# Kernel optimization log

Hardware: AMD Instinct MI355X
Metric: run time of the kernel (lower is better)

## Reference

```python
import jax, jax.numpy as jnp
import numpy as np

N = 10000       # nodes (cells)
NFEAT = 2000    # gene-expression features
NFE = 256       # embed features
NH = 128        # nhid
NHE = 64        # nhid_embed
L = 2           # gcn_hid_layers_num
NOUT = 20       # output classes
BN_EPS = 1e-5


def bn_eval(x, g, b, rm, rv):
    # BatchNorm1d in eval mode: affine with running stats
    return g * (x - rm) / jnp.sqrt(rv + BN_EPS) + b


def lstm_layer(seq, Wih, Whh, bih, bhh):
    # seq: [T, N, H_in]; PyTorch gate order i, f, g, o
    Hd = Whh.shape[1]
    def step(carry, xt):
        h, c = carry
        z = xt @ Wih.T + h @ Whh.T + bih + bhh  # [N, 4H]
        i, f, g, o = jnp.split(z, 4, axis=1)
        c = jax.nn.sigmoid(f) * c + jax.nn.sigmoid(i) * jnp.tanh(g)
        h = jax.nn.sigmoid(o) * jnp.tanh(c)
        return (h, c), h
    h0 = jnp.zeros((seq.shape[1], Hd), seq.dtype)
    _, hs = jax.lax.scan(step, (h0, h0), seq)
    return hs  # [T, N, H]


def setup_inputs() -> dict:
    key = jax.random.key(0)
    ks = iter(jax.random.split(key, 48))
    def rn(shape, scale=1.0):
        return jax.random.normal(next(ks), shape, dtype=jnp.float32) * scale
    inp = {}
    inp["x"] = rn((N, NFEAT))
    inp["embed"] = rn((N, NFE))
    inp["adj"] = jax.random.uniform(next(ks), (N, N), dtype=jnp.float32)
    inp["W_in"] = rn((NH, NFEAT), NFEAT ** -0.5); inp["b_in"] = jnp.zeros((NH,), jnp.float32)
    inp["bn_in_g"] = jnp.ones((NH,), jnp.float32); inp["bn_in_b"] = jnp.zeros((NH,), jnp.float32)
    inp["bn_in_rm"] = rn((NH,), 0.1); inp["bn_in_rv"] = jnp.ones((NH,), jnp.float32)
    # gs_block: Linear(2*nhid -> nhid) per layer (concat self + mean-aggregated neighbors)
    inp["W_gs"] = rn((L, NH, 2 * NH), (2 * NH) ** -0.5); inp["b_gs"] = jnp.zeros((L, NH), jnp.float32)
    for l in range(2):  # 2-layer LSTM jumping-knowledge
        inp[f"Wih{l}"] = rn((4 * NH, NH), NH ** -0.5)
        inp[f"Whh{l}"] = rn((4 * NH, NH), NH ** -0.5)
        inp[f"bih{l}"] = jnp.zeros((4 * NH,), jnp.float32)
        inp[f"bhh{l}"] = jnp.zeros((4 * NH,), jnp.float32)
    inp["W_emb"] = rn((NHE, NFE), NFE ** -0.5); inp["b_emb"] = jnp.zeros((NHE,), jnp.float32)
    inp["bn_emb_g"] = jnp.ones((NHE,), jnp.float32); inp["bn_emb_b"] = jnp.zeros((NHE,), jnp.float32)
    inp["bn_emb_rm"] = rn((NHE,), 0.1); inp["bn_emb_rv"] = jnp.ones((NHE,), jnp.float32)
    D = NH + NHE
    inp["W_fc"] = rn((D, D), D ** -0.5); inp["b_fc"] = jnp.zeros((D,), jnp.float32)
    inp["bn_fc_g"] = jnp.ones((D,), jnp.float32); inp["bn_fc_b"] = jnp.zeros((D,), jnp.float32)
    inp["bn_fc_rm"] = rn((D,), 0.1); inp["bn_fc_rv"] = jnp.ones((D,), jnp.float32)
    inp["W_out"] = rn((NOUT, D), D ** -0.5); inp["b_out"] = jnp.zeros((NOUT,), jnp.float32)
    return inp


def _forward(x, embed, adj, W_in, b_in, bn_in_g, bn_in_b, bn_in_rm, bn_in_rv,
             W_gs, b_gs, Wih0, Whh0, bih0, bhh0, Wih1, Whh1, bih1, bhh1,
             W_emb, b_emb, bn_emb_g, bn_emb_b, bn_emb_rm, bn_emb_rv,
             W_fc, b_fc, bn_fc_g, bn_fc_b, bn_fc_rm, bn_fc_rv, W_out, b_out):
    # input projection + BN + ELU (dropout: eval mode -> no-op)
    h = jax.nn.elu(bn_eval(x @ W_in.T + b_in, bn_in_g, bn_in_b, bn_in_rm, bn_in_rv))
    # GraphSAGE mean aggregator: row-normalized dense adjacency
    adj_norm = adj / adj.sum(1, keepdims=True)
    jk = []
    for l in range(L):
        neigh = adj_norm @ h                              # [N, NH] neighbor mean
        comb = jnp.concatenate([h, neigh], axis=1)        # [N, 2NH] (gcn=False)
        h = jax.nn.relu(comb @ W_gs[l].T + b_gs[l])
        h = h / jnp.maximum(jnp.linalg.norm(h, axis=1, keepdims=True), 1e-12)  # F.normalize
        jk.append(h)
    seq = jnp.stack(jk, 0)                                # [L, N, NH]
    hs = lstm_layer(seq, Wih0, Whh0, bih0, bhh0)
    hs = lstm_layer(hs, Wih1, Whh1, bih1, bhh1)
    h = hs.mean(0)                                        # JK: mean of LSTM outputs
    h = jax.nn.elu(bn_eval(h, bn_in_g, bn_in_b, bn_in_rm, bn_in_rv))  # bn_node_in_exp reused
    e = jax.nn.elu(bn_eval(embed @ W_emb.T + b_emb, bn_emb_g, bn_emb_b, bn_emb_rm, bn_emb_rv))
    h = jnp.concatenate([h, e], axis=1)                   # [N, NH+NHE]
    h = jax.nn.elu(bn_eval(h @ W_fc.T + b_fc, bn_fc_g, bn_fc_b, bn_fc_rm, bn_fc_rv))
    logits = h @ W_out.T + b_out
    return jax.nn.log_softmax(logits, axis=1)


def reference(x, embed, adj, W_in, b_in, bn_in_g, bn_in_b, bn_in_rm, bn_in_rv,
              W_gs, b_gs, Wih0, Whh0, bih0, bhh0, Wih1, Whh1, bih1, bhh1,
              W_emb, b_emb, bn_emb_g, bn_emb_b, bn_emb_rm, bn_emb_rv,
              W_fc, b_fc, bn_fc_g, bn_fc_b, bn_fc_rm, bn_fc_rv, W_out, b_out):
    return _forward(x, embed, adj, W_in, b_in, bn_in_g, bn_in_b, bn_in_rm, bn_in_rv,
                    W_gs, b_gs, Wih0, Whh0, bih0, bhh0, Wih1, Whh1, bih1, bhh1,
                    W_emb, b_emb, bn_emb_g, bn_emb_b, bn_emb_rm, bn_emb_rv,
                    W_fc, b_fc, bn_fc_g, bn_fc_b, bn_fc_rm, bn_fc_rv, W_out, b_out)
```

## Files before the change

### kernel.cpp

```cpp
#include <hip/hip_runtime.h>
#include <hip/hip_bf16.h>
#include <math.h>

#define N_NODES 10000
#define NFEAT   2000
#define NFE     256
#define NH      128
#define NHE     64
#define NOUT    20
#define DCAT    192
#define BN_EPS  1e-5f

#define KP      10016
#define KSTEPS  313
#define MT      157
#define NSPLIT  8
#define KC      40
#define MPAD    10048

typedef __attribute__((ext_vector_type(8))) short  bf16x8;
typedef __attribute__((ext_vector_type(4))) float  f32x4;

__device__ __forceinline__ float sigm(float x) { return 1.0f / (1.0f + expf(-x)); }

__device__ __forceinline__ unsigned short f2bf(float x) {
    union { __hip_bfloat16 h; unsigned short u; } c;
    c.h = __float2bfloat16(x);
    return c.u;
}

__device__ __forceinline__ bf16x8 cvt8(const float* v) {
    bf16x8 r;
    #pragma unroll
    for (int i = 0; i < 8; ++i) r[i] = (short)f2bf(v[i]);
    return r;
}

__global__ __launch_bounds__(256) void htrans_kernel(const float* __restrict__ h,
                                                     unsigned short* __restrict__ hT)
{
    __shared__ float t[32][36];
    const int k0 = blockIdx.x * 32, c0 = blockIdx.y * 32;
    {
        int r = threadIdx.x >> 3, ci = threadIdx.x & 7;
        int kg = k0 + r;
        float4 v = {0.f, 0.f, 0.f, 0.f};
        if (kg < N_NODES) v = *(const float4*)(h + (size_t)kg * NH + c0 + ci * 4);
        t[r][ci * 4 + 0] = v.x; t[r][ci * 4 + 1] = v.y;
        t[r][ci * 4 + 2] = v.z; t[r][ci * 4 + 3] = v.w;
    }
    __syncthreads();
    {
        int c = threadIdx.x >> 3, ki = threadIdx.x & 7;
        ushort4 o;
        o.x = f2bf(t[ki * 4 + 0][c]); o.y = f2bf(t[ki * 4 + 1][c]);
        o.z = f2bf(t[ki * 4 + 2][c]); o.w = f2bf(t[ki * 4 + 3][c]);
        *(ushort4*)(hT + (size_t)(c0 + c) * KP + k0 + ki * 4) = o;
    }
}

__global__ __launch_bounds__(256) void adjmm_kernel(const float* __restrict__ adj,
                                                    const unsigned short* __restrict__ hT,
                                                    float* __restrict__ part,
                                                    float* __restrict__ part_s)
{
    __shared__ unsigned short sa[64 * 32];
    __shared__ unsigned short sb[128 * 32];
    const int tid  = threadIdx.x;
    const int lane = tid & 63, w = tid >> 6;
    const int m0   = blockIdx.x * 64;
    const int ks0  = blockIdx.y * KC;
    const int ks1  = min(ks0 + KC, KSTEPS);
    const int r0   = (w & 1) * 32;
    const int c0   = (w >> 1) * 64;

    const int arow = tid >> 2, agrp = tid & 3;
    const size_t abase = (size_t)min(m0 + arow, N_NODES - 1) * N_NODES;
    const int bcol = tid >> 1, bg0 = (tid & 1) * 2;

    float rs = 0.f;
// ... 32 lines not shown
            int g   = lane >> 4;
            av[rb] = *(const bf16x8*)(sa + row * 32 + ((g ^ (row & 3)) << 3));
        }
        #pragma unroll
        for (int cb = 0; cb < 4; ++cb) {
            int col = c0 + cb * 16 + (lane & 15);
            int g   = lane >> 4;
            bv[cb] = *(const bf16x8*)(sb + col * 32 + ((g ^ (col & 3)) << 3));
        }
        #pragma unroll
        for (int rb = 0; rb < 2; ++rb)
            #pragma unroll
            for (int cb = 0; cb < 4; ++cb)
                acc[rb][cb] = __builtin_amdgcn_mfma_f32_16x16x32_bf16(av[rb], bv[cb],
                                                                      acc[rb][cb], 0, 0, 0);
    }

    rs += __shfl_xor(rs, 1);
    rs += __shfl_xor(rs, 2);
    if ((tid & 3) == 0) part_s[(size_t)blockIdx.y * MPAD + m0 + arow] = rs;

    float* pout = part + (size_t)blockIdx.y * MPAD * NH;
    #pragma unroll
    for (int rb = 0; rb < 2; ++rb) {
        #pragma unroll
        for (int cb = 0; cb < 4; ++cb) {
            int rowb = m0 + r0 + rb * 16 + (lane >> 4) * 4;
            int col  = c0 + cb * 16 + (lane & 15);
            #pragma unroll
            for (int reg = 0; reg < 4; ++reg)
                pout[(size_t)(rowb + reg) * NH + col] = acc[rb][cb][reg];
        }
    }
}

__global__ __launch_bounds__(256) void sinv_kernel(const float* __restrict__ part_s,
                                                   float* __restrict__ sinv)
{
    int m = blockIdx.x * 256 + threadIdx.x;
    if (m >= N_NODES) return;
    float a = 0.f;
    #pragma unroll
    for (int c = 0; c < NSPLIT; ++c) a += part_s[(size_t)c * MPAD + m];
    sinv[m] = 1.0f / a;
}

__global__ __launch_bounds__(256) void nreduce_kernel(const float* __restrict__ part,
                                                      const float* __restrict__ sinv,
                                                      float* __restrict__ neigh)
{
    int idx = blockIdx.x * 256 + threadIdx.x;
    if (idx >= N_NODES * NH / 4) return;
    const int m = idx >> 5;
    const size_t ch = (size_t)MPAD * NH / 4;
    const float4* p = (const float4*)part;
    float a0 = 0.f, a1 = 0.f, a2 = 0.f, a3 = 0.f;
    #pragma unroll
    for (int c = 0; c < NSPLIT; ++c) {
        float4 v = p[c * ch + idx];
        a0 += v.x; a1 += v.y; a2 += v.z; a3 += v.w;
    }
    const float inv = sinv[m];
    float4 o; o.x = a0 * inv; o.y = a1 * inv; o.z = a2 * inv; o.w = a3 * inv;
    *(float4*)(neigh + (size_t)idx * 4) = o;
}

__global__ __launch_bounds__(256) void xw_mfma_kernel(const float* __restrict__ x,
                                                      const float* __restrict__ Wn,
                                                      float* __restrict__ part)
{
    __shared__ unsigned short sa[64 * 32];
    __shared__ unsigned short sb[128 * 32];
    const int tid  = threadIdx.x;
    const int lane = tid & 63, w = tid >> 6;
    const int m0   = blockIdx.x * 64;
    const int TOT  = (NFEAT + 31) / 32;
    const int s0   = blockIdx.y * 8;
    const int s1   = min(s0 + 8, TOT);
    const int r0   = (w & 1) * 32;
    const int c0   = (w >> 1) * 64;

    const int arow = tid >> 2, agrp = tid & 3;
    const size_t abase = (size_t)min(m0 + arow, N_NODES - 1) * NFEAT;

    f32x4 acc[2][4];
    #pragma unroll
    for (int i = 0; i < 2; ++i)
        #pragma unroll
        for (int j = 0; j < 4; ++j) acc[i][j] = (f32x4){0.f, 0.f, 0.f, 0.f};

    for (int ks = s0; ks < s1; ++ks) {
        const int k0 = ks * 32;
        float av8[8], bv8[2][8];
        {
            const int kg = k0 + agrp * 8;
            if (kg + 8 <= NFEAT) {
                float4 u0 = *(const float4*)(x + abase + kg);
                float4 u1 = *(const float4*)(x + abase + kg + 4);
                av8[0]=u0.x; av8[1]=u0.y; av8[2]=u0.z; av8[3]=u0.w;
                av8[4]=u1.x; av8[5]=u1.y; av8[6]=u1.z; av8[7]=u1.w;
            } else {
// ... 44 lines not shown
            for (int cb = 0; cb < 4; ++cb)
                acc[rb][cb] = __builtin_amdgcn_mfma_f32_16x16x32_bf16(av[rb], bv[cb],
                                                                      acc[rb][cb], 0, 0, 0);
    }
    float* pout = part + (size_t)blockIdx.y * MPAD * NH;
    #pragma unroll
    for (int rb = 0; rb < 2; ++rb)
        #pragma unroll
        for (int cb = 0; cb < 4; ++cb) {
            int rowb = m0 + r0 + rb * 16 + (lane >> 4) * 4;
            int col  = c0 + cb * 16 + (lane & 15);
            #pragma unroll
            for (int reg = 0; reg < 4; ++reg)
                pout[(size_t)(rowb + reg) * NH + col] = acc[rb][cb][reg];
        }
}

__global__ __launch_bounds__(256) void xw_reduce_kernel(const float* __restrict__ part,
                                                        const float* __restrict__ bias,
                                                        const float* __restrict__ g,
                                                        const float* __restrict__ bb,
                                                        const float* __restrict__ rm,
                                                        const float* __restrict__ rv,
                                                        float* __restrict__ h)
{
    int idx = blockIdx.x * 256 + threadIdx.x;
    if (idx >= N_NODES * NH / 4) return;
    const int c4 = (idx & 31) * 4;
    const size_t ch = (size_t)MPAD * NH / 4;
    const float4* p = (const float4*)part;
    float a[4] = {0.f, 0.f, 0.f, 0.f};
    #pragma unroll
    for (int c = 0; c < NSPLIT; ++c) {
        float4 v = p[c * ch + idx];
        a[0] += v.x; a[1] += v.y; a[2] += v.z; a[3] += v.w;
    }
    float o[4];
    #pragma unroll
    for (int j = 0; j < 4; ++j) {
        int c = c4 + j;
        float sc = g[c] / sqrtf(rv[c] + BN_EPS);
        float t = (a[j] + bias[c] - rm[c]) * sc + bb[c];
        o[j] = t > 0.f ? t : expm1f(t);
    }
    float4 ov; ov.x = o[0]; ov.y = o[1]; ov.z = o[2]; ov.w = o[3];
    *(float4*)(h + (size_t)idx * 4) = ov;
}

template<int BM, int BN, int EPI>
__global__ __launch_bounds__(256) void wgemm_mfma_kernel(
    int M, int K, int kSplitA,
    const float* __restrict__ a1, int lda1,
    const float* __restrict__ a2, int lda2,
    int kSplitB,
    const float* __restrict__ b1, int ldb1,
    const float* __restrict__ b2, int ldb2,
    float* __restrict__ out, int ldo,
    const float* __restrict__ bias1, const float* __restrict__ bias2,
    const float* __restrict__ bng, const float* __restrict__ bnb,
    const float* __restrict__ bnrm, const float* __restrict__ bnrv)
{
    constexpr int WC = BN / 64;
    constexpr int WR = 4 / WC;
    static_assert(WR * WC == 4 && BM == WR * 32, "geometry");
    constexpr int NGA = BM * 4 / 256;
    constexpr int NGB = BN * 4 / 256;
    __shared__ unsigned short sa[BM * 32];
    __shared__ unsigned short sb[BN * 32];
    const int tid  = threadIdx.x;
    const int lane = tid & 63, w = tid >> 6;
    const int m0   = blockIdx.x * BM, n0 = blockIdx.y * BN;
    const int r0   = (w % WR) * 32, c0 = (w / WR) * 64;

    f32x4 acc[2][4];
    #pragma unroll
    for (int i = 0; i < 2; ++i)
        #pragma unroll
        for (int j = 0; j < 4; ++j) acc[i][j] = (f32x4){0.f, 0.f, 0.f, 0.f};

    for (int k0 = 0; k0 < K; k0 += 32) {
        float ar[NGA][8], br[NGB][8];
        #pragma unroll
        for (int t = 0; t < NGA; ++t) {
            int gidx = tid + t * 256;
            int row = gidx >> 2, grp = gidx & 3;
            int mg = min(m0 + row, M - 1);
            int kg = k0 + grp * 8;
            const float* src = (kg < kSplitA) ? (a1 + (size_t)mg * lda1 + kg)
                                              : (a2 + (size_t)mg * lda2 + (kg - kSplitA));
            float4 u0 = *(const float4*)src;
            float4 u1 = *(const float4*)(src + 4);
            ar[t][0]=u0.x; ar[t][1]=u0.y; ar[t][2]=u0.z; ar[t][3]=u0.w;
            ar[t][4]=u1.x; ar[t][5]=u1.y; ar[t][6]=u1.z; ar[t][7]=u1.w;
        }
        #pragma unroll
        for (int t = 0; t < NGB; ++t) {
            int gidx = tid + t * 256;
            int n = gidx >> 2, grp = gidx & 3;
            int ng = n0 + n;
            int kg = k0 + grp * 8;
            const float* src = (kg < kSplitB) ? (b1 + (size_t)ng * ldb1 + kg)
                                              : (b2 + (size_t)ng * ldb2 + (kg - kSplitB));
            float4 u0 = *(const float4*)src;
            float4 u1 = *(const float4*)(src + 4);
            br[t][0]=u0.x; br[t][1]=u0.y; br[t][2]=u0.z; br[t][3]=u0.w;
            br[t][4]=u1.x; br[t][5]=u1.y; br[t][6]=u1.z; br[t][7]=u1.w;
        }
        __syncthreads();
        #pragma unroll
        for (int t = 0; t < NGA; ++t) {
            int gidx = tid + t * 256;
            int row = gidx >> 2, grp = gidx & 3;
            *(bf16x8*)(sa + row * 32 + ((grp ^ (row & 3)) << 3)) = cvt8(ar[t]);
        }
        #pragma unroll
        for (int t = 0; t < NGB; ++t) {
            int gidx = tid + t * 256;
            int n = gidx >> 2, grp = gidx & 3;
            *(bf16x8*)(sb + n * 32 + ((grp ^ (n & 3)) << 3)) = cvt8(br[t]);
        }
        __syncthreads();
        bf16x8 av[2], bv[4];
        #pragma unroll
        for (int rb = 0; rb < 2; ++rb) {
            int row = r0 + rb * 16 + (lane & 15);
            int g   = lane >> 4;
            av[rb] = *(const bf16x8*)(sa + row * 32 + ((g ^ (row & 3)) << 3));
        }
        #pragma unroll
        for (int cb = 0; cb < 4; ++cb) {
            int col = c0 + cb * 16 + (lane & 15);
            int g   = lane >> 4;
            bv[cb] = *(const bf16x8*)(sb + col * 32 + ((g ^ (col & 3)) << 3));
        }
        #pragma unroll
        for (int rb = 0; rb < 2; ++rb)
            #pragma unroll
            for (int cb = 0; cb < 4; ++cb)
                acc[rb][cb] = __builtin_amdgcn_mfma_f32_16x16x32_bf16(av[rb], bv[cb],
                                                                      acc[rb][cb], 0, 0, 0);
    }

    #pragma unroll
    for (int cb = 0; cb < 4; ++cb) {
        const int colg = n0 + c0 + cb * 16 + (lane & 15);
        float badd = bias1[colg];
        if constexpr (EPI == 0) badd += bias2[colg];
        float sc = 0.f, sh = 0.f;
        if constexpr (EPI == 1) {
            sc = bng[colg] / sqrtf(bnrv[colg] + BN_EPS);
            sh = bnb[colg] - bnrm[colg] * sc;
        }
        #pragma unroll
        for (int rb = 0; rb < 2; ++rb) {
            int rowb = m0 + r0 + rb * 16 + (lane >> 4) * 4;
            #pragma unroll
            for (int reg = 0; reg < 4; ++reg) {
                int m = rowb + reg;
                if (m < M) {
                    float t = acc[rb][cb][reg] + badd;
                    if constexpr (EPI == 1) {
                        t = t * sc + sh;
                        t = t > 0.f ? t : expm1f(t);
                    }
                    if constexpr (EPI == 2) t = fmaxf(t, 0.f);
                    out[(size_t)m * ldo + colg] = t;
                }
            }
        }
    }
}

__global__ __launch_bounds__(256) void rownorm_kernel(const float* __restrict__ in,
                                                      float* __restrict__ out)
{
    const int w = threadIdx.x >> 6, lane = threadIdx.x & 63;
    const int r = blockIdx.x * 4 + w;
    float2 v = ((const float2*)(in + (size_t)r * NH))[lane];
    float ss = v.x * v.x + v.y * v.y;
    #pragma unroll
    for (int msk = 32; msk >= 1; msk >>= 1) ss += __shfl_xor(ss, msk);
    float sc = 1.0f / fmaxf(sqrtf(ss), 1e-12f);
    float2 o; o.x = v.x * sc; o.y = v.y * sc;
    ((float2*)(out + (size_t)r * NH))[lane] = o;
}

template<bool HASC>
__global__ __launch_bounds__(256) void lstm_gate_kernel(const float* __restrict__ z,
                                                        const float* __restrict__ cprev,
                                                        float* __restrict__ hout,
                                                        float* __restrict__ cout)
{
    int idx = blockIdx.x * 256 + threadIdx.x;
    if (idx >= N_NODES * NH / 4) return;
    int m = idx >> 5, c4 = (idx & 31) * 4;
    const float* zr = z + (size_t)m * 512 + c4;
    float4 zi = *(const float4*)(zr);
    float4 zf = *(const float4*)(zr + 128);
    float4 zg = *(const float4*)(zr + 256);
    float4 zo = *(const float4*)(zr + 384);
    float4 cp = {0.f, 0.f, 0.f, 0.f};
    if (HASC) cp = *(const float4*)(cprev + (size_t)m * NH + c4);
    float zia[4] = {zi.x, zi.y, zi.z, zi.w};
    float zfa[4] = {zf.x, zf.y, zf.z, zf.w};
    float zga[4] = {zg.x, zg.y, zg.z, zg.w};
    float zoa[4] = {zo.x, zo.y, zo.z, zo.w};
    float cpa[4] = {cp.x, cp.y, cp.z, cp.w};
    float ho[4], co[4];
    #pragma unroll
    for (int j = 0; j < 4; ++j) {
        float ig = sigm(zia[j]);
        float gg = tanhf(zga[j]);
        float cn = ig * gg;
        if (HASC) cn += sigm(zfa[j]) * cpa[j];
        co[j] = cn;
        ho[j] = sigm(zoa[j]) * tanhf(cn);
    }
    float4 hv; hv.x = ho[0]; hv.y = ho[1]; hv.z = ho[2]; hv.w = ho[3];
    float4 cv; cv.x = co[0]; cv.y = co[1]; cv.z = co[2]; cv.w = co[3];
    *(float4*)(hout + (size_t)m * NH + c4) = hv;
    *(float4*)(cout + (size_t)m * NH + c4) = cv;
}

__global__ __launch_bounds__(256) void jkmean_bnelu_kernel(const float* __restrict__ a,
                                                           const float* __restrict__ b,
                                                           const float* __restrict__ g,
                                                           const float* __restrict__ bb,
                                                           const float* __restrict__ rm,
                                                           const float* __restrict__ rv,
                                                           float* __restrict__ out)
{
    int idx = blockIdx.x * 256 + threadIdx.x;
    if (idx >= N_NODES * NH / 4) return;
    int c4 = (idx & 31) * 4;
    float4 va = *(const float4*)(a + (size_t)idx * 4);
    float4 vb = *(const float4*)(b + (size_t)idx * 4);
    float av[4] = {va.x, va.y, va.z, va.w};
    float bv[4] = {vb.x, vb.y, vb.z, vb.w};
    float o[4];
    #pragma unroll
    for (int j = 0; j < 4; ++j) {
        int c = c4 + j;
        float t = 0.5f * (av[j] + bv[j]);
        float sc = g[c] / sqrtf(rv[c] + BN_EPS);
        t = (t - rm[c]) * sc + bb[c];
        o[j] = t > 0.f ? t : expm1f(t);
    }
    float4 ov; ov.x = o[0]; ov.y = o[1]; ov.z = o[2]; ov.w = o[3];
    *(float4*)(out + (size_t)idx * 4) = ov;
}

__global__ __launch_bounds__(256) void out_kernel(const float* __restrict__ hfc,
                                                  const float* __restrict__ W_out,
                                                  const float* __restrict__ b_out,
                                                  float* __restrict__ out)
{
    __shared__ float wl[NOUT * 193];
    __shared__ float rl[4][DCAT];
    const int tid = threadIdx.x;
    for (int i = tid; i < NOUT * DCAT; i += 256)
        wl[(i / DCAT) * 193 + (i % DCAT)] = W_out[i];
    const int w = tid >> 6, lane = tid & 63;
    const int r = blockIdx.x * 4 + w;
    for (int k = lane; k < DCAT; k += 64) rl[w][k] = hfc[(size_t)r * DCAT + k];
    __syncthreads();
    const int c = lane;
    float acc = -INFINITY;
    if (c < NOUT) {
        acc = b_out[c];
        #pragma unroll 4
        for (int k = 0; k < DCAT; ++k) acc += rl[w][k] * wl[c * 193 + k];
    }
// ... 35 lines not shown
    const float* bn_e_g  = (const float*)d_in[21];
    const float* bn_e_b  = (const float*)d_in[22];
    const float* bn_e_rm = (const float*)d_in[23];
    const float* bn_e_rv = (const float*)d_in[24];
    const float* W_fc    = (const float*)d_in[25];
    const float* b_fc    = (const float*)d_in[26];
    const float* bn_f_g  = (const float*)d_in[27];
    const float* bn_f_b  = (const float*)d_in[28];
    const float* bn_f_rm = (const float*)d_in[29];
    const float* bn_f_rv = (const float*)d_in[30];
    const float* W_out   = (const float*)d_in[31];
    const float* b_out   = (const float*)d_in[32];
    float* outp = (float*)d_out;

    const size_t HB = (size_t)N_NODES * NH * sizeof(float);
    char* wp = (char*)d_ws;
    auto carve = [&](size_t bytes) {
        void* p = (void*)wp;
        wp += (bytes + 1023) & ~(size_t)1023;
        return p;
    };
    float* part  = (float*)carve((size_t)NSPLIT * MPAD * NH * sizeof(float));
    float* part_s= (float*)carve((size_t)NSPLIT * MPAD * sizeof(float));
    float* sinv  = (float*)carve(N_NODES * sizeof(float));
    float* h_in  = (float*)carve(HB);
    float* neigh = (float*)carve(HB);
    float* jkraw = (float*)carve(HB);
    float* jk0   = (float*)carve(HB);
    float* jk1   = (float*)carve(HB);
    float* h1_0  = (float*)carve(HB);
    float* h1_1  = (float*)carve(HB);
    float* c1    = (float*)carve(HB);
    float* h2_0  = (float*)carve(HB);
    float* h2_1  = (float*)carve(HB);
    float* c2    = (float*)carve(HB);
    float* hpost = (float*)carve(HB);
    float* z     = (float*)carve((size_t)N_NODES * 512 * sizeof(float));
    float* e     = (float*)carve((size_t)N_NODES * NHE * sizeof(float));
    float* hfc   = (float*)carve((size_t)N_NODES * DCAT * sizeof(float));
    unsigned short* hT = (unsigned short*)carve((size_t)NH * KP * 2);
    if ((size_t)(wp - (char*)d_ws) > ws_size) return;

    const dim3 blk(256);

    xw_mfma_kernel<<<dim3(MT, 8), blk, 0, stream>>>(x, W_in, part);
    xw_reduce_kernel<<<1250, blk, 0, stream>>>(part, b_in, bn_in_g, bn_in_b,
                                               bn_in_rm, bn_in_rv, h_in);

    htrans_kernel<<<dim3(KSTEPS, 4), blk, 0, stream>>>(h_in, hT);
    adjmm_kernel<<<dim3(MT, NSPLIT), blk, 0, stream>>>(adj, hT, part, part_s);
    sinv_kernel<<<40, blk, 0, stream>>>(part_s, sinv);
    nreduce_kernel<<<1250, blk, 0, stream>>>(part, sinv, neigh);
    wgemm_mfma_kernel<64, 128, 2><<<dim3(MT, 1), blk, 0, stream>>>(
        N_NODES, 2 * NH, NH, h_in, NH, neigh, NH,
        2 * NH, W_gs, 2 * NH, nullptr, 0,
        jkraw, NH, b_gs, nullptr, nullptr, nullptr, nullptr, nullptr);
    rownorm_kernel<<<2500, blk, 0, stream>>>(jkraw, jk0);

    htrans_kernel<<<dim3(KSTEPS, 4), blk, 0, stream>>>(jk0, hT);
    adjmm_kernel<<<dim3(MT, NSPLIT), blk, 0, stream>>>(adj, hT, part, part_s);
    sinv_kernel<<<40, blk, 0, stream>>>(part_s, sinv);
    nreduce_kernel<<<1250, blk, 0, stream>>>(part, sinv, neigh);
    wgemm_mfma_kernel<64, 128, 2><<<dim3(MT, 1), blk, 0, stream>>>(
        N_NODES, 2 * NH, NH, jk0, NH, neigh, NH,
        2 * NH, W_gs + 128 * 256, 2 * NH, nullptr, 0,
        jkraw, NH, b_gs + 128, nullptr, nullptr, nullptr, nullptr, nullptr);
    rownorm_kernel<<<2500, blk, 0, stream>>>(jkraw, jk1);

    wgemm_mfma_kernel<64, 128, 0><<<dim3(MT, 4), blk, 0, stream>>>(
        N_NODES, NH, NH, jk0, NH, nullptr, 0,
        NH, Wih0, NH, nullptr, 0,
        z, 4 * NH, bih0, bhh0, nullptr, nullptr, nullptr, nullptr);
    lstm_gate_kernel<false><<<1250, blk, 0, stream>>>(z, nullptr, h1_0, c1);
    wgemm_mfma_kernel<64, 128, 0><<<dim3(MT, 4), blk, 0, stream>>>(
        N_NODES, 2 * NH, NH, jk1, NH, h1_0, NH,
        NH, Wih0, NH, Whh0, NH,
        z, 4 * NH, bih0, bhh0, nullptr, nullptr, nullptr, nullptr);
    lstm_gate_kernel<true><<<1250, blk, 0, stream>>>(z, c1, h1_1, c1);
    wgemm_mfma_kernel<64, 128, 0><<<dim3(MT, 4), blk, 0, stream>>>(
        N_NODES, NH, NH, h1_0, NH, nullptr, 0,
        NH, Wih1, NH, nullptr, 0,
        z, 4 * NH, bih1, bhh1, nullptr, nullptr, nullptr, nullptr);
    lstm_gate_kernel<false><<<1250, blk, 0, stream>>>(z, nullptr, h2_0, c2);
    wgemm_mfma_kernel<64, 128, 0><<<dim3(MT, 4), blk, 0, stream>>>(
        N_NODES, 2 * NH, NH, h1_1, NH, h2_0, NH,
        NH, Wih1, NH, Whh1, NH,
        z, 4 * NH, bih1, bhh1, nullptr, nullptr, nullptr, nullptr);
    lstm_gate_kernel<true><<<1250, blk, 0, stream>>>(z, c2, h2_1, c2);

    jkmean_bnelu_kernel<<<1250, blk, 0, stream>>>(h2_0, h2_1, bn_in_g, bn_in_b,
                                                  bn_in_rm, bn_in_rv, hpost);

    wgemm_mfma_kernel<128, 64, 1><<<dim3(79, 1), blk, 0, stream>>>(
        N_NODES, NFE, NFE, embed, NFE, nullptr, 0,
        NFE, W_emb, NFE, nullptr, 0,
        e, NHE, b_emb, nullptr, bn_e_g, bn_e_b, bn_e_rm, bn_e_rv);

    wgemm_mfma_kernel<128, 64, 1><<<dim3(79, 3), blk, 0, stream>>>(
        N_NODES, DCAT, NH, hpost, NH, e, NHE,
        DCAT, W_fc, DCAT, nullptr, 0,
        hfc, DCAT, b_fc, nullptr, bn_f_g, bn_f_b, bn_f_rm, bn_f_rv);

    out_kernel<<<2500, blk, 0, stream>>>(hfc, W_out, b_out, outp);
}
```

Measured before the change: 521.7 us.

## Fuse LSTM gemm+gates, GraphSAGE gemm+rownorm+transpose, and prune auxiliary kernels

Replaces separate gemm, gate, rownorm, transpose and sinv kernels with fused kernels. The LSTM GEMM and gate math run in one kernel using pre-converted bf16 weights, the GS GEMM fuses ReLU, L2 row norm and the bf16 transpose for the next adjacency matmul, and the xw reduce emits the transposed bf16 copy. The xw split count is halved and the degree inverse is folded into nreduce. This removes the large z round-trip and several launches, at the cost of higher per-block register and LDS use plus a weight conversion launch.

Result: faster. 486.2 us (-6.8%).

```diff
diff --git a/kernel.cpp b/kernel.cpp
--- a/kernel.cpp
+++ b/kernel.cpp
@@ -16,6 +16,7 @@
 #define MT      157
 #define NSPLIT  8
 #define KC      40
+#define NSPLX   4
 #define MPAD    10048
 
 typedef __attribute__((ext_vector_type(8))) short  bf16x8;
@@ -36,26 +37,27 @@
     return r;
 }
 
-__global__ __launch_bounds__(256) void htrans_kernel(const float* __restrict__ h,
-                                                     unsigned short* __restrict__ hT)
-{
-    __shared__ float t[32][36];
-    const int k0 = blockIdx.x * 32, c0 = blockIdx.y * 32;
-    {
-        int r = threadIdx.x >> 3, ci = threadIdx.x & 7;
-        int kg = k0 + r;
-        float4 v = {0.f, 0.f, 0.f, 0.f};
-        if (kg < N_NODES) v = *(const float4*)(h + (size_t)kg * NH + c0 + ci * 4);
-        t[r][ci * 4 + 0] = v.x; t[r][ci * 4 + 1] = v.y;
-        t[r][ci * 4 + 2] = v.z; t[r][ci * 4 + 3] = v.w;
-    }
-    __syncthreads();
-    {
-        int c = threadIdx.x >> 3, ki = threadIdx.x & 7;
-        ushort4 o;
-        o.x = f2bf(t[ki * 4 + 0][c]); o.y = f2bf(t[ki * 4 + 1][c]);
-        o.z = f2bf(t[ki * 4 + 2][c]); o.w = f2bf(t[ki * 4 + 3][c]);
-        *(ushort4*)(hT + (size_t)(c0 + c) * KP + k0 + ki * 4) = o;
+__global__ __launch_bounds__(256) void wconv_kernel(const float* __restrict__ Wih0,
+                                                    const float* __restrict__ Whh0,
+                                                    const float* __restrict__ Wih1,
+                                                    const float* __restrict__ Whh1,
+                                                    const float* __restrict__ Wgs,
+                                                    unsigned short* __restrict__ wl,
+                                                    unsigned short* __restrict__ wgb)
+{
+    const int total = 262144 + 65536;
+    for (int i = blockIdx.x * 256 + threadIdx.x; i < total; i += gridDim.x * 256) {
+        if (i < 262144) {
+            int l = i >> 17, rem = i & 131071;
+            int n = rem >> 8, k = rem & 255;
+            const float* src;
+            if (l == 0) src = (k < 128) ? (Wih0 + n * 128 + k) : (Whh0 + n * 128 + (k - 128));
+            else        src = (k < 128) ? (Wih1 + n * 128 + k) : (Whh1 + n * 128 + (k - 128));
+            wl[i] = f2bf(*src);
+        } else {
+            int j = i - 262144;
+            wgb[j] = f2bf(Wgs[j]);
+        }
     }
 }
 
@@ -134,7 +136,7 @@
 
     float* pout = part + (size_t)blockIdx.y * MPAD * NH;
     #pragma unroll
-    for (int rb = 0; rb < 2; ++rb) {
+    for (int rb = 0; rb < 2; ++rb)
         #pragma unroll
         for (int cb = 0; cb < 4; ++cb) {
             int rowb = m0 + r0 + rb * 16 + (lane >> 4) * 4;
@@ -143,27 +145,24 @@
             for (int reg = 0; reg < 4; ++reg)
                 pout[(size_t)(rowb + reg) * NH + col] = acc[rb][cb][reg];
         }
-    }
-}
-
-__global__ __launch_bounds__(256) void sinv_kernel(const float* __restrict__ part_s,
-                                                   float* __restrict__ sinv)
-{
-    int m = blockIdx.x * 256 + threadIdx.x;
-    if (m >= N_NODES) return;
-    float a = 0.f;
-    #pragma unroll
-    for (int c = 0; c < NSPLIT; ++c) a += part_s[(size_t)c * MPAD + m];
-    sinv[m] = 1.0f / a;
 }
 
 __global__ __launch_bounds__(256) void nreduce_kernel(const float* __restrict__ part,
-                                                      const float* __restrict__ sinv,
+                                                      const float* __restrict__ part_s,
                                                       float* __restrict__ neigh)
 {
     int idx = blockIdx.x * 256 + threadIdx.x;
     if (idx >= N_NODES * NH / 4) return;
     const int m = idx >> 5;
+    const int lane = threadIdx.x & 63;
+    float inv = 0.f;
+    if ((lane & 31) == 0) {
+        float a = 0.f;
+        #pragma unroll
+        for (int c = 0; c < NSPLIT; ++c) a += part_s[(size_t)c * MPAD + m];
+        inv = 1.0f / a;
+    }
+    inv = __shfl(inv, lane & 32);
     const size_t ch = (size_t)MPAD * NH / 4;
     const float4* p = (const float4*)part;
     float a0 = 0.f, a1 = 0.f, a2 = 0.f, a3 = 0.f;
@@ -172,7 +171,6 @@
         float4 v = p[c * ch + idx];
         a0 += v.x; a1 += v.y; a2 += v.z; a3 += v.w;
     }
-    const float inv = sinv[m];
     float4 o; o.x = a0 * inv; o.y = a1 * inv; o.z = a2 * inv; o.w = a3 * inv;
     *(float4*)(neigh + (size_t)idx * 4) = o;
 }
@@ -187,8 +185,8 @@
     const int lane = tid & 63, w = tid >> 6;
     const int m0   = blockIdx.x * 64;
     const int TOT  = (NFEAT + 31) / 32;
-    const int s0   = blockIdx.y * 8;
-    const int s1   = min(s0 + 8, TOT);
+    const int s0   = blockIdx.y * 16;
+    const int s1   = min(s0 + 16, TOT);
     const int r0   = (w & 1) * 32;
     const int c0   = (w >> 1) * 64;
 
@@ -279,16 +277,20 @@
                                                         const float* __restrict__ bb,
                                                         const float* __restrict__ rm,
                                                         const float* __restrict__ rv,
-                                                        float* __restrict__ h)
-{
-    int idx = blockIdx.x * 256 + threadIdx.x;
-    if (idx >= N_NODES * NH / 4) return;
-    const int c4 = (idx & 31) * 4;
+                                                        float* __restrict__ h,
+                                                        unsigned short* __restrict__ hT)
+{
+    __shared__ unsigned short tb[128][8];
+    const int tid = threadIdx.x;
+    int idx = blockIdx.x * 256 + tid;
+    const int c4 = (tid & 31) * 4;
+    const int lr = tid >> 5;
+    const int m0g = blockIdx.x * 8;
     const size_t ch = (size_t)MPAD * NH / 4;
     const float4* p = (const float4*)part;
     float a[4] = {0.f, 0.f, 0.f, 0.f};
     #pragma unroll
-    for (int c = 0; c < NSPLIT; ++c) {
+    for (int c = 0; c < NSPLX; ++c) {
         float4 v = p[c * ch + idx];
         a[0] += v.x; a[1] += v.y; a[2] += v.z; a[3] += v.w;
     }
@@ -299,21 +301,286 @@
         float sc = g[c] / sqrtf(rv[c] + BN_EPS);
         float t = (a[j] + bias[c] - rm[c]) * sc + bb[c];
         o[j] = t > 0.f ? t : expm1f(t);
+        tb[c][lr] = f2bf(o[j]);
     }
     float4 ov; ov.x = o[0]; ov.y = o[1]; ov.z = o[2]; ov.w = o[3];
     *(float4*)(h + (size_t)idx * 4) = ov;
-}
-
-template<int BM, int BN, int EPI>
-__global__ __launch_bounds__(256) void wgemm_mfma_kernel(
+    __syncthreads();
+    if (tid < 128) {
+        ushort4 v0, v1;
+        v0.x = tb[tid][0]; v0.y = tb[tid][1]; v0.z = tb[tid][2]; v0.w = tb[tid][3];
+        v1.x = tb[tid][4]; v1.y = tb[tid][5]; v1.z = tb[tid][6]; v1.w = tb[tid][7];
+        *(ushort4*)(hT + (size_t)tid * KP + m0g)     = v0;
+        *(ushort4*)(hT + (size_t)tid * KP + m0g + 4) = v1;
+        if (blockIdx.x == 0) {
+            ushort4 zz; zz.x = zz.y = zz.z = zz.w = 0;
+            #pragma unroll
+            for (int q = 0; q < 4; ++q)
+                *(ushort4*)(hT + (size_t)tid * KP + 10000 + q * 4) = zz;
+        }
+    }
+}
+
+template<bool WRITE_T>
+__global__ __launch_bounds__(256) void gs_fused_kernel(const float* __restrict__ h,
+                                                       const float* __restrict__ neigh,
+                                                       const unsigned short* __restrict__ Wg,
+                                                       const float* __restrict__ bg,
+                                                       float* __restrict__ jk,
+                                                       unsigned short* __restrict__ jkT)
+{
+    __shared__ unsigned short sa[64 * 32];
+    __shared__ unsigned short sb[128 * 32];
+    __shared__ float ssq_l[64][2];
+    __shared__ unsigned short tb[WRITE_T ? 128 * 64 : 1];
+    const int tid  = threadIdx.x;
+    const int lane = tid & 63, w = tid >> 6;
+    const int m0   = blockIdx.x * 64;
+    const int r0   = (w & 1) * 32;
+    const int c0   = (w >> 1) * 64;
+    const int arow = tid >> 2, agrp = tid & 3;
+    const int mg   = min(m0 + arow, N_NODES - 1);
+
+    f32x4 acc[2][4];
+    #pragma unroll
+    for (int i = 0; i < 2; ++i)
+        #pragma unroll
+        for (int j = 0; j < 4; ++j) acc[i][j] = (f32x4){0.f, 0.f, 0.f, 0.f};
+
+    for (int k0 = 0; k0 < 256; k0 += 32) {
+        const int kg = k0 + agrp * 8;
+        const float* asrc = (kg < 128) ? (h + (size_t)mg * NH + kg)
+                                       : (neigh + (size_t)mg * NH + (kg - 128));
+        float4 u0 = *(const float4*)asrc;
+        float4 u1 = *(const float4*)(asrc + 4);
+        float a8[8] = {u0.x, u0.y, u0.z, u0.w, u1.x, u1.y, u1.z, u1.w};
+        bf16x8 b8[2];
+        #pragma unroll
+        for (int t = 0; t < 2; ++t) {
+            int gi = tid + t * 256;
+            int n = gi >> 2, grp = gi & 3;
+            b8[t] = *(const bf16x8*)(Wg + (size_t)n * 256 + k0 + grp * 8);
+        }
+        __syncthreads();
+        *(bf16x8*)(sa + arow * 32 + ((agrp ^ (arow & 3)) << 3)) = cvt8(a8);
+        #pragma unroll
+        for (int t = 0; t < 2; ++t) {
+            int gi = tid + t * 256;
+            int n = gi >> 2, grp = gi & 3;
+            *(bf16x8*)(sb + n * 32 + ((grp ^ (n & 3)) << 3)) = b8[t];
+        }
+        __syncthreads();
+        bf16x8 av[2], bv[4];
+        #pragma unroll
+        for (int rb = 0; rb < 2; ++rb) {
+            int row = r0 + rb * 16 + (lane & 15);
+            int g   = lane >> 4;
+            av[rb] = *(const bf16x8*)(sa + row * 32 + ((g ^ (row & 3)) << 3));
+        }
+        #pragma unroll
+        for (int cb = 0; cb < 4; ++cb) {
+            int col = c0 + cb * 16 + (lane & 15);
+            int g   = lane >> 4;
+            bv[cb] = *(const bf16x8*)(sb + col * 32 + ((g ^ (col & 3)) << 3));
+        }
+        #pragma unroll
+        for (int rb = 0; rb < 2; ++rb)
+            #pragma unroll
+            for (int cb = 0; cb < 4; ++cb)
+                acc[rb][cb] = __builtin_amdgcn_mfma_f32_16x16x32_bf16(av[rb], bv[cb],
+                                                                      acc[rb][cb], 0, 0, 0);
+    }
+
+    float vv[2][4][4];
+    float ps[2][4] = {};
+    #pragma unroll
+    for (int rb = 0; rb < 2; ++rb)
+        #pragma unroll
+        for (int cb = 0; cb < 4; ++cb) {
+            int colg = c0 + cb * 16 + (lane & 15);
+            float b = bg[colg];
+            #pragma unroll
+            for (int reg = 0; reg < 4; ++reg) {
+                float t = fmaxf(acc[rb][cb][reg] + b, 0.f);
+                vv[rb][cb][reg] = t;
+                ps[rb][reg] += t * t;
+            }
+        }
+    #pragma unroll
+    for (int msk = 1; msk < 16; msk <<= 1)
+        #pragma unroll
+        for (int rb = 0; rb < 2; ++rb)
+            #pragma unroll
+            for (int reg = 0; reg < 4; ++reg)
+                ps[rb][reg] += __shfl_xor(ps[rb][reg], msk);
+    if ((lane & 15) == 0) {
+        #pragma unroll
+        for (int rb = 0; rb < 2; ++rb)
+            #pragma unroll
+            for (int reg = 0; reg < 4; ++reg)
+                ssq_l[r0 + rb * 16 + (lane >> 4) * 4 + reg][w >> 1] = ps[rb][reg];
+    }
+    __syncthreads();
+    #pragma unroll
+    for (int rb = 0; rb < 2; ++rb)
+        #pragma unroll
+        for (int reg = 0; reg < 4; ++reg) {
+            int lr = r0 + rb * 16 + (lane >> 4) * 4 + reg;
+            float s = ssq_l[lr][0] + ssq_l[lr][1];
+            float sc = 1.0f / fmaxf(sqrtf(s), 1e-12f);
+            int m = m0 + lr;
+            #pragma unroll
+            for (int cb = 0; cb < 4; ++cb) {
+                int colg = c0 + cb * 16 + (lane & 15);
+                float o = vv[rb][cb][reg] * sc;
+                if (m < N_NODES) jk[(size_t)m * NH + colg] = o;
+                if constexpr (WRITE_T) tb[colg * 64 + lr] = f2bf(o);
+            }
+        }
+    if constexpr (WRITE_T) {
+        __syncthreads();
+        #pragma unroll
+        for (int p = 0; p < 4; ++p) {
+            int flat = (tid + p * 256) * 8;
+            int c = flat >> 6, mo = flat & 63;
+            int kglob = m0 + mo;
+            if (kglob < KP) {
+                unsigned short tmp[8];
+                #pragma unroll
+                for (int i = 0; i < 8; ++i)
+                    tmp[i] = (kglob + i < N_NODES) ? tb[c * 64 + mo + i] : (unsigned short)0;
+                ushort4 v0, v1;
+                v0.x = tmp[0]; v0.y = tmp[1]; v0.z = tmp[2]; v0.w = tmp[3];
+                v1.x = tmp[4]; v1.y = tmp[5]; v1.z = tmp[6]; v1.w = tmp[7];
+                *(ushort4*)(jkT + (size_t)c * KP + kglob)     = v0;
+                *(ushort4*)(jkT + (size_t)c * KP + kglob + 4) = v1;
+            }
+        }
+    }
+}
+
+template<bool HASC, bool FINAL>
+__global__ __launch_bounds__(256) void lstm_fused_kernel(
+    int K, const float* __restrict__ a1, const float* __restrict__ a2,
+    const unsigned short* __restrict__ wl,
+    const float* __restrict__ bih, const float* __restrict__ bhh,
+    const float* __restrict__ cprev,
+    float* __restrict__ hout, float* __restrict__ cout,
+    const float* __restrict__ hmean, const float* __restrict__ bng,
+    const float* __restrict__ bnb, const float* __restrict__ bnrm,
+    const float* __restrict__ bnrv, float* __restrict__ hpost)
+{
+    __shared__ unsigned short sa[32 * 32];
+    __shared__ unsigned short sb[512 * 32];
+    const int tid  = threadIdx.x;
+    const int lane = tid & 63, w = tid >> 6;
+    const int m0   = blockIdx.x * 32;
+    const int arow = tid >> 2, agrp = tid & 3;
+    const int mg   = min(m0 + arow, N_NODES - 1);
+
+    f32x4 acc[2][8];
+    #pragma unroll
+    for (int i = 0; i < 2; ++i)
+        #pragma unroll
+        for (int j = 0; j < 8; ++j) acc[i][j] = (f32x4){0.f, 0.f, 0.f, 0.f};
+
+    for (int k0 = 0; k0 < K; k0 += 32) {
+        float a8[8];
+        if (tid < 128) {
+            int kg = k0 + agrp * 8;
+            const float* asrc = (kg < 128) ? (a1 + (size_t)mg * NH + kg)
+                                           : (a2 + (size_t)mg * NH + (kg - 128));
+            float4 u0 = *(const float4*)asrc;
+            float4 u1 = *(const float4*)(asrc + 4);
+            a8[0]=u0.x; a8[1]=u0.y; a8[2]=u0.z; a8[3]=u0.w;
+            a8[4]=u1.x; a8[5]=u1.y; a8[6]=u1.z; a8[7]=u1.w;
+        }
+        bf16x8 b8[8];
+        #pragma unroll
+        for (int t = 0; t < 8; ++t) {
+            int gi = tid + t * 256;
+            int n = gi >> 2, grp = gi & 3;
+            b8[t] = *(const bf16x8*)(wl + (size_t)n * 256 + k0 + grp * 8);
+        }
+        __syncthreads();
+        if (tid < 128)
+            *(bf16x8*)(sa + arow * 32 + ((agrp ^ (arow & 3)) << 3)) = cvt8(a8);
+        #pragma unroll
+        for (int t = 0; t < 8; ++t) {
+            int gi = tid + t * 256;
+            int n = gi >> 2, grp = gi & 3;
+            *(bf16x8*)(sb + n * 32 + ((grp ^ (n & 3)) << 3)) = b8[t];
+        }
+        __syncthreads();
+        bf16x8 av[2];
+        #pragma unroll
+        for (int rb = 0; rb < 2; ++rb) {
+            int row = rb * 16 + (lane & 15);
+            int g   = lane >> 4;
+            av[rb] = *(const bf16x8*)(sa + row * 32 + ((g ^ (row & 3)) << 3));
+        }
+        #pragma unroll
+        for (int gate = 0; gate < 4; ++gate)
+            #pragma unroll
+            for (int cb = 0; cb < 2; ++cb) {
+                int col = gate * 128 + w * 32 + cb * 16 + (lane & 15);
+                int g   = lane >> 4;
+                bf16x8 bv = *(const bf16x8*)(sb + col * 32 + ((g ^ (col & 3)) << 3));
+                #pragma unroll
+                for (int rb = 0; rb < 2; ++rb)
+                    acc[rb][gate * 2 + cb] =
+                        __builtin_amdgcn_mfma_f32_16x16x32_bf16(av[rb], bv,
+                                                                acc[rb][gate * 2 + cb], 0, 0, 0);
+            }
+    }
+
+    #pragma unroll
+    for (int cb = 0; cb < 2; ++cb) {
+        const int cg = w * 32 + cb * 16 + (lane & 15);
+        const float bi = bih[0 * 128 + cg] + bhh[0 * 128 + cg];
+        const float bf = bih[1 * 128 + cg] + bhh[1 * 128 + cg];
+        const float bgg= bih[2 * 128 + cg] + bhh[2 * 128 + cg];
+        const float bo = bih[3 * 128 + cg] + bhh[3 * 128 + cg];
+        float sc = 0.f, sh = 0.f;
+        if constexpr (FINAL) {
+            sc = bng[cg] / sqrtf(bnrv[cg] + BN_EPS);
+            sh = bnb[cg] - bnrm[cg] * sc;
+        }
+        #pragma unroll
+        for (int rb = 0; rb < 2; ++rb) {
+            #pragma unroll
+            for (int reg = 0; reg < 4; ++reg) {
+                int m = m0 + rb * 16 + (lane >> 4) * 4 + reg;
+                if (m < N_NODES) {
+                    float zi = acc[rb][0 + cb][reg] + bi;
+                    float zf = acc[rb][2 + cb][reg] + bf;
+                    float zg = acc[rb][4 + cb][reg] + bgg;
+                    float zo = acc[rb][6 + cb][reg] + bo;
+                    float cn = sigm(zi) * tanhf(zg);
+                    if constexpr (HASC) cn += sigm(zf) * cprev[(size_t)m * NH + cg];
+                    float hv = sigm(zo) * tanhf(cn);
+                    if constexpr (FINAL) {
+                        float t = 0.5f * (hmean[(size_t)m * NH + cg] + hv);
+                        t = t * sc + sh;
+                        hpost[(size_t)m * NH + cg] = t > 0.f ? t : expm1f(t);
+                    } else {
+                        hout[(size_t)m * NH + cg] = hv;
+                        cout[(size_t)m * NH + cg] = cn;
+                    }
+                }
+            }
+        }
+    }
+}
+
+template<int BM, int BN>
+__global__ __launch_bounds__(256) void wgemm_bnelu_kernel(
     int M, int K, int kSplitA,
     const float* __restrict__ a1, int lda1,
     const float* __restrict__ a2, int lda2,
-    int kSplitB,
-    const float* __restrict__ b1, int ldb1,
-    const float* __restrict__ b2, int ldb2,
+    const float* __restrict__ B, int ldb, int ncol,
     float* __restrict__ out, int ldo,
-    const float* __restrict__ bias1, const float* __restrict__ bias2,
+    const float* __restrict__ bias,
     const float* __restrict__ bng, const float* __restrict__ bnb,
     const float* __restrict__ bnrm, const float* __restrict__ bnrv)
 {
@@ -339,8 +606,8 @@
         float ar[NGA][8], br[NGB][8];
         #pragma unroll
         for (int t = 0; t < NGA; ++t) {
-            int gidx = tid + t * 256;
-            int row = gidx >> 2, grp = gidx & 3;
+            int gi = tid + t * 256;
+            int row = gi >> 2, grp = gi & 3;
             int mg = min(m0 + row, M - 1);
             int kg = k0 + grp * 8;
             const float* src = (kg < kSplitA) ? (a1 + (size_t)mg * lda1 + kg)
@@ -352,12 +619,11 @@
         }
         #pragma unroll
         for (int t = 0; t < NGB; ++t) {
-            int gidx = tid + t * 256;
-            int n = gidx >> 2, grp = gidx & 3;
-            int ng = n0 + n;
+            int gi = tid + t * 256;
+            int n = gi >> 2, grp = gi & 3;
+            int ng = min(n0 + n, ncol - 1);
             int kg = k0 + grp * 8;
-            const float* src = (kg < kSplitB) ? (b1 + (size_t)ng * ldb1 + kg)
-                                              : (b2 + (size_t)ng * ldb2 + (kg - kSplitB));
+            const float* src = B + (size_t)ng * ldb + kg;
             float4 u0 = *(const float4*)src;
             float4 u1 = *(const float4*)(src + 4);
             br[t][0]=u0.x; br[t][1]=u0.y; br[t][2]=u0.z; br[t][3]=u0.w;
@@ -366,14 +632,14 @@
         __syncthreads();
         #pragma unroll
         for (int t = 0; t < NGA; ++t) {
-            int gidx = tid + t * 256;
-            int row = gidx >> 2, grp = gidx & 3;
+            int gi = tid + t * 256;
+            int row = gi >> 2, grp = gi & 3;
             *(bf16x8*)(sa + row * 32 + ((grp ^ (row & 3)) << 3)) = cvt8(ar[t]);
         }
         #pragma unroll
         for (int t = 0; t < NGB; ++t) {
-            int gidx = tid + t * 256;
-            int n = gidx >> 2, grp = gidx & 3;
+            int gi = tid + t * 256;
+            int n = gi >> 2, grp = gi & 3;
             *(bf16x8*)(sb + n * 32 + ((grp ^ (n & 3)) << 3)) = cvt8(br[t]);
         }
         __syncthreads();
@@ -401,110 +667,23 @@
     #pragma unroll
     for (int cb = 0; cb < 4; ++cb) {
         const int colg = n0 + c0 + cb * 16 + (lane & 15);
-        float badd = bias1[colg];
-        if constexpr (EPI == 0) badd += bias2[colg];
-        float sc = 0.f, sh = 0.f;
-        if constexpr (EPI == 1) {
-            sc = bng[colg] / sqrtf(bnrv[colg] + BN_EPS);
-            sh = bnb[colg] - bnrm[colg] * sc;
-        }
+        const int cc = min(colg, ncol - 1);
+        float badd = bias[cc];
+        float sc = bng[cc] / sqrtf(bnrv[cc] + BN_EPS);
+        float sh = bnb[cc] - bnrm[cc] * sc;
         #pragma unroll
         for (int rb = 0; rb < 2; ++rb) {
             int rowb = m0 + r0 + rb * 16 + (lane >> 4) * 4;
             #pragma unroll
             for (int reg = 0; reg < 4; ++reg) {
                 int m = rowb + reg;
-                if (m < M) {
-                    float t = acc[rb][cb][reg] + badd;
-                    if constexpr (EPI == 1) {
-                        t = t * sc + sh;
-                        t = t > 0.f ? t : expm1f(t);
-                    }
-                    if constexpr (EPI == 2) t = fmaxf(t, 0.f);
-                    out[(size_t)m * ldo + colg] = t;
+                if (m < M && colg < ncol) {
+                    float t = (acc[rb][cb][reg] + badd) * sc + sh;
+                    out[(size_t)m * ldo + colg] = t > 0.f ? t : expm1f(t);
                 }
             }
         }
     }
-}
-
-__global__ __launch_bounds__(256) void rownorm_kernel(const float* __restrict__ in,
-                                                      float* __restrict__ out)
-{
-    const int w = threadIdx.x >> 6, lane = threadIdx.x & 63;
-    const int r = blockIdx.x * 4 + w;
-    float2 v = ((const float2*)(in + (size_t)r * NH))[lane];
-    float ss = v.x * v.x + v.y * v.y;
-    #pragma unroll
-    for (int msk = 32; msk >= 1; msk >>= 1) ss += __shfl_xor(ss, msk);
-    float sc = 1.0f / fmaxf(sqrtf(ss), 1e-12f);
-    float2 o; o.x = v.x * sc; o.y = v.y * sc;
-    ((float2*)(out + (size_t)r * NH))[lane] = o;
-}
-
-template<bool HASC>
-__global__ __launch_bounds__(256) void lstm_gate_kernel(const float* __restrict__ z,
-                                                        const float* __restrict__ cprev,
-                                                        float* __restrict__ hout,
-                                                        float* __restrict__ cout)
-{
-    int idx = blockIdx.x * 256 + threadIdx.x;
-    if (idx >= N_NODES * NH / 4) return;
-    int m = idx >> 5, c4 = (idx & 31) * 4;
-    const float* zr = z + (size_t)m * 512 + c4;
-    float4 zi = *(const float4*)(zr);
-    float4 zf = *(const float4*)(zr + 128);
-    float4 zg = *(const float4*)(zr + 256);
-    float4 zo = *(const float4*)(zr + 384);
-    float4 cp = {0.f, 0.f, 0.f, 0.f};
-    if (HASC) cp = *(const float4*)(cprev + (size_t)m * NH + c4);
-    float zia[4] = {zi.x, zi.y, zi.z, zi.w};
-    float zfa[4] = {zf.x, zf.y, zf.z, zf.w};
-    float zga[4] = {zg.x, zg.y, zg.z, zg.w};
-    float zoa[4] = {zo.x, zo.y, zo.z, zo.w};
-    float cpa[4] = {cp.x, cp.y, cp.z, cp.w};
-    float ho[4], co[4];
-    #pragma unroll
-    for (int j = 0; j < 4; ++j) {
-        float ig = sigm(zia[j]);
-        float gg = tanhf(zga[j]);
-        float cn = ig * gg;
-        if (HASC) cn += sigm(zfa[j]) * cpa[j];
-        co[j] = cn;
-        ho[j] = sigm(zoa[j]) * tanhf(cn);
-    }
-    float4 hv; hv.x = ho[0]; hv.y = ho[1]; hv.z = ho[2]; hv.w = ho[3];
-    float4 cv; cv.x = co[0]; cv.y = co[1]; cv.z = co[2]; cv.w = co[3];
-    *(float4*)(hout + (size_t)m * NH + c4) = hv;
-    *(float4*)(cout + (size_t)m * NH + c4) = cv;
-}
-
-__global__ __launch_bounds__(256) void jkmean_bnelu_kernel(const float* __restrict__ a,
-                                                           const float* __restrict__ b,
-                                                           const float* __restrict__ g,
-                                                           const float* __restrict__ bb,
-                                                           const float* __restrict__ rm,
-                                                           const float* __restrict__ rv,
-                                                           float* __restrict__ out)
-{
-    int idx = blockIdx.x * 256 + threadIdx.x;
-    if (idx >= N_NODES * NH / 4) return;
-    int c4 = (idx & 31) * 4;
-    float4 va = *(const float4*)(a + (size_t)idx * 4);
-    float4 vb = *(const float4*)(b + (size_t)idx * 4);
-    float av[4] = {va.x, va.y, va.z, va.w};
-    float bv[4] = {vb.x, vb.y, vb.z, vb.w};
-    float o[4];
-    #pragma unroll
-    for (int j = 0; j < 4; ++j) {
-        int c = c4 + j;
-        float t = 0.5f * (av[j] + bv[j]);
-        float sc = g[c] / sqrtf(rv[c] + BN_EPS);
-        t = (t - rm[c]) * sc + bb[c];
-        o[j] = t > 0.f ? t : expm1f(t);
-    }
-    float4 ov; ov.x = o[0]; ov.y = o[1]; ov.z = o[2]; ov.w = o[3];
-    *(float4*)(out + (size_t)idx * 4) = ov;
 }
 
 __global__ __launch_bounds__(256) void out_kernel(const float* __restrict__ hfc,
@@ -586,84 +765,62 @@
     };
     float* part  = (float*)carve((size_t)NSPLIT * MPAD * NH * sizeof(float));
     float* part_s= (float*)carve((size_t)NSPLIT * MPAD * sizeof(float));
-    float* sinv  = (float*)carve(N_NODES * sizeof(float));
     float* h_in  = (float*)carve(HB);
     float* neigh = (float*)carve(HB);
-    float* jkraw = (float*)carve(HB);
     float* jk0   = (float*)carve(HB);
     float* jk1   = (float*)carve(HB);
     float* h1_0  = (float*)carve(HB);
     float* h1_1  = (float*)carve(HB);
     float* c1    = (float*)carve(HB);
     float* h2_0  = (float*)carve(HB);
-    float* h2_1  = (float*)carve(HB);
     float* c2    = (float*)carve(HB);
     float* hpost = (float*)carve(HB);
-    float* z     = (float*)carve((size_t)N_NODES * 512 * sizeof(float));
     float* e     = (float*)carve((size_t)N_NODES * NHE * sizeof(float));
     float* hfc   = (float*)carve((size_t)N_NODES * DCAT * sizeof(float));
-    unsigned short* hT = (unsigned short*)carve((size_t)NH * KP * 2);
+    unsigned short* hT  = (unsigned short*)carve((size_t)NH * KP * 2);
+    unsigned short* wl  = (unsigned short*)carve((size_t)2 * 512 * 256 * 2);
+    unsigned short* wgb = (unsigned short*)carve((size_t)2 * 128 * 256 * 2);
     if ((size_t)(wp - (char*)d_ws) > ws_size) return;
 
     const dim3 blk(256);
 
-    xw_mfma_kernel<<<dim3(MT, 8), blk, 0, stream>>>(x, W_in, part);
+    wconv_kernel<<<320, blk, 0, stream>>>(Wih0, Whh0, Wih1, Whh1, W_gs, wl, wgb);
+
+    xw_mfma_kernel<<<dim3(MT, NSPLX), blk, 0, stream>>>(x, W_in, part);
     xw_reduce_kernel<<<1250, blk, 0, stream>>>(part, b_in, bn_in_g, bn_in_b,
-                                               bn_in_rm, bn_in_rv, h_in);
-
-    htrans_kernel<<<dim3(KSTEPS, 4), blk, 0, stream>>>(h_in, hT);
+                                               bn_in_rm, bn_in_rv, h_in, hT);
+
     adjmm_kernel<<<dim3(MT, NSPLIT), blk, 0, stream>>>(adj, hT, part, part_s);
-    sinv_kernel<<<40, blk, 0, stream>>>(part_s, sinv);
-    nreduce_kernel<<<1250, blk, 0, stream>>>(part, sinv, neigh);
-    wgemm_mfma_kernel<64, 128, 2><<<dim3(MT, 1), blk, 0, stream>>>(
-        N_NODES, 2 * NH, NH, h_in, NH, neigh, NH,
-        2 * NH, W_gs, 2 * NH, nullptr, 0,
-        jkraw, NH, b_gs, nullptr, nullptr, nullptr, nullptr, nullptr);
-    rownorm_kernel<<<2500, blk, 0, stream>>>(jkraw, jk0);
-
-    htrans_kernel<<<dim3(KSTEPS, 4), blk, 0, stream>>>(jk0, hT);
+    nreduce_kernel<<<1250, blk, 0, stream>>>(part, part_s, neigh);
+    gs_fused_kernel<true><<<MT, blk, 0, stream>>>(h_in, neigh, wgb, b_gs, jk0, hT);
+
     adjmm_kernel<<<dim3(MT, NSPLIT), blk, 0, stream>>>(adj, hT, part, part_s);
-    sinv_kernel<<<40, blk, 0, stream>>>(part_s, sinv);
-    nreduce_kernel<<<1250, blk, 0, stream>>>(part, sinv, neigh);
-    wgemm_mfma_kernel<64, 128, 2><<<dim3(MT, 1), blk, 0, stream>>>(
-        N_NODES, 2 * NH, NH, jk0, NH, neigh, NH,
-        2 * NH, W_gs + 128 * 256, 2 * NH, nullptr, 0,
-        jkraw, NH, b_gs + 128, nullptr, nullptr, nullptr, nullptr, nullptr);
-    rownorm_kernel<<<2500, blk, 0, stream>>>(jkraw, jk1);
-
-    wgemm_mfma_kernel<64, 128, 0><<<dim3(MT, 4), blk, 0, stream>>>(
-        N_NODES, NH, NH, jk0, NH, nullptr, 0,
-        NH, Wih0, NH, nullptr, 0,
-        z, 4 * NH, bih0, bhh0, nullptr, nullptr, nullptr, nullptr);
-    lstm_gate_kernel<false><<<1250, blk, 0, stream>>>(z, nullptr, h1_0, c1);
-    wgemm_mfma_kernel<64, 128, 0><<<dim3(MT, 4), blk, 0, stream>>>(
-        N_NODES, 2 * NH, NH, jk1, NH, h1_0, NH,
-        NH, Wih0, NH, Whh0, NH,
-        z, 4 * NH, bih0, bhh0, nullptr, nullptr, nullptr, nullptr);
-    lstm_gate_kernel<true><<<1250, blk, 0, stream>>>(z, c1, h1_1, c1);
-    wgemm_mfma_kernel<64, 128, 0><<<dim3(MT, 4), blk, 0, stream>>>(
-        N_NODES, NH, NH, h1_0, NH, nullptr, 0,
-        NH, Wih1, NH, nullptr, 0,
-        z, 4 * NH, bih1, bhh1, nullptr, nullptr, nullptr, nullptr);
-    lstm_gate_kernel<false><<<1250, blk, 0, stream>>>(z, nullptr, h2_0, c2);
-    wgemm_mfma_kernel<64, 128, 0><<<dim3(MT, 4), blk, 0, stream>>>(
-        N_NODES, 2 * NH, NH, h1_1, NH, h2_0, NH,
-        NH, Wih1, NH, Whh1, NH,
-        z, 4 * NH, bih1, bhh1, nullptr, nullptr, nullptr, nullptr);
-    lstm_gate_kernel<true><<<1250, blk, 0, stream>>>(z, c2, h2_1, c2);
-
-    jkmean_bnelu_kernel<<<1250, blk, 0, stream>>>(h2_0, h2_1, bn_in_g, bn_in_b,
-                                                  bn_in_rm, bn_in_rv, hpost);
-
-    wgemm_mfma_kernel<128, 64, 1><<<dim3(79, 1), blk, 0, stream>>>(
+    nreduce_kernel<<<1250, blk, 0, stream>>>(part, part_s, neigh);
+    gs_fused_kernel<false><<<MT, blk, 0, stream>>>(jk0, neigh, wgb + 128 * 256, b_gs + 128,
+                                                   jk1, nullptr);
+
+    lstm_fused_kernel<false, false><<<313, blk, 0, stream>>>(
+        128, jk0, jk0, wl, bih0, bhh0, nullptr, h1_0, c1,
+        nullptr, nullptr, nullptr, nullptr, nullptr, nullptr);
+    lstm_fused_kernel<true, false><<<313, blk, 0, stream>>>(
+        256, jk1, h1_0, wl, bih0, bhh0, c1, h1_1, c1,
+        nullptr, nullptr, nullptr, nullptr, nullptr, nullptr);
+    lstm_fused_kernel<false, false><<<313, blk, 0, stream>>>(
+        128, h1_0, h1_0, wl + 512 * 256, bih1, bhh1, nullptr, h2_0, c2,
+        nullptr, nullptr, nullptr, nullptr, nullptr, nullptr);
+    lstm_fused_kernel<true, true><<<313, blk, 0, stream>>>(
+        256, h1_1, h2_0, wl + 512 * 256, bih1, bhh1, c2, nullptr, nullptr,
+        h2_0, bn_in_g, bn_in_b, bn_in_rm, bn_in_rv, hpost);
+
+    wgemm_bnelu_kernel<64, 128><<<dim3(MT, 1), blk, 0, stream>>>(
         N_NODES, NFE, NFE, embed, NFE, nullptr, 0,
-        NFE, W_emb, NFE, nullptr, 0,
-        e, NHE, b_emb, nullptr, bn_e_g, bn_e_b, bn_e_rm, bn_e_rv);
-
-    wgemm_mfma_kernel<128, 64, 1><<<dim3(79, 3), blk, 0, stream>>>(
+        W_emb, NFE, NHE, e, NHE,
+        b_emb, bn_e_g, bn_e_b, bn_e_rm, bn_e_rv);
+
+    wgemm_bnelu_kernel<64, 128><<<dim3(MT, 2), blk, 0, stream>>>(
         N_NODES, DCAT, NH, hpost, NH, e, NHE,
-        DCAT, W_fc, DCAT, nullptr, 0,
-        hfc, DCAT, b_fc, nullptr, bn_f_g, bn_f_b, bn_f_rm, bn_f_rv);
+        W_fc, DCAT, DCAT, hfc, DCAT,
+        b_fc, bn_f_g, bn_f_b, bn_f_rm, bn_f_rv);
 
     out_kernel<<<2500, blk, 0, stream>>>(hfc, W_out, b_out, outp);
 }
```
